# Optimization experiments

Hardware: AMD Instinct MI355X
Metric: run time of the kernel (lower is better)

Reference implementation:

```python
import jax, jax.numpy as jnp
import numpy as np


def setup_inputs() -> dict:
    key = jax.random.key(0)
    kK, kQ = jax.random.split(key)
    B, S, D = 8, 2048, 512
    K = jax.random.normal(kK, (B, S, D), dtype=jnp.float32)
    Q = jax.random.normal(kQ, (B, S, D), dtype=jnp.float32)
    return {"K": K, "Q": Q}


def reference(K, Q):
    # K: [B, S_k, D], Q: [B, S_q, D]
    S_q = Q.shape[1]
    S_k = K.shape[1]
    # Causal mask: -inf strictly above the diagonal (k=1), as in np.triu(..., k=1)
    mask = jnp.where(jnp.triu(jnp.ones((S_q, S_k), dtype=bool), k=1), -jnp.inf, 0.0).astype(jnp.float32)
    # NOTE: original scales by sqrt(window_size_keys) (seq len), and adds mask BEFORE scaling.
    logits = (jnp.einsum('bqd,bkd->bqk', Q, K) + mask) / jnp.sqrt(jnp.float32(S_k))
    return jax.nn.softmax(logits, axis=-1)
```

## Files before the change

### kernel.cpp

```cpp
#include <hip/hip_runtime.h>
#include <hip/hip_bf16.h>
#include <math.h>

#define B_SZ 8
#define SEQ 2048
#define DIM 512
#define NT (SEQ / 128)
#define NTRI (NT * (NT + 1) / 2)

typedef __attribute__((ext_vector_type(8))) short bf16x8;
typedef __attribute__((ext_vector_type(8))) unsigned short u16x8;
typedef __attribute__((ext_vector_type(4))) float f32x4;

#define GLOBAL_AS __attribute__((address_space(1)))
#define LDS_AS __attribute__((address_space(3)))

__device__ __forceinline__ unsigned short f2bf(float f) {
    unsigned int u = __builtin_bit_cast(unsigned int, f);
    u += 0x7fffu + ((u >> 16) & 1u);
    return (unsigned short)(u >> 16);
}

__device__ __forceinline__ void load_lds16(const void* g, void* l) {
    __builtin_amdgcn_global_load_lds((const GLOBAL_AS unsigned int*)g,
                                     (LDS_AS unsigned int*)l, 16, 0, 0);
}

__global__ __launch_bounds__(256)
void convert_kernel(const float* __restrict__ Qs, const float* __restrict__ Ks,
                    unsigned short* __restrict__ Qd, unsigned short* __restrict__ Kd) {
    const float* src = blockIdx.y ? Qs : Ks;
    unsigned short* dst = blockIdx.y ? Qd : Kd;
    const int base = blockIdx.x * (256 * 8) + threadIdx.x;
    const float4* s = (const float4*)src;
#pragma unroll
    for (int j = 0; j < 8; j++) {
        int i = base + j * 256;
        float4 a = s[2 * i];
        float4 b = s[2 * i + 1];
        u16x8 o;
        o[0] = f2bf(a.x); o[1] = f2bf(a.y); o[2] = f2bf(a.z); o[3] = f2bf(a.w);
        o[4] = f2bf(b.x); o[5] = f2bf(b.y); o[6] = f2bf(b.z); o[7] = f2bf(b.w);
        ((u16x8*)dst)[i] = o;
    }
}

#define BM 128
#define BK 32
__global__ __launch_bounds__(256)
void logits_exp(const unsigned short* __restrict__ Qb, const unsigned short* __restrict__ Kb,
                float* __restrict__ out, float* __restrict__ partials) {
    const int tid = blockIdx.x;
    const int b = blockIdx.y;
    int tq = (int)((sqrtf(8.f * (float)tid + 1.f) - 1.f) * 0.5f);
    while ((tq + 1) * (tq + 2) / 2 <= tid) tq++;
    while (tq * (tq + 1) / 2 > tid) tq--;
    const int tk = tid - tq * (tq + 1) / 2;

    __shared__ __align__(16) unsigned short a_lds[BM * BK];
    __shared__ __align__(16) unsigned short b_lds[BM * BK];

    const int t = threadIdx.x;
    const int wave = t >> 6;
    const int lane = t & 63;
    const int l16 = lane & 15;
    const int quad = lane >> 4;
    const int wm = wave >> 1;
    const int wn = wave & 1;

    const unsigned short* Qrow = Qb + ((size_t)b * SEQ + (size_t)tq * BM) * DIM;
    const unsigned short* Krow = Kb + ((size_t)b * SEQ + (size_t)tk * BM) * DIM;

    const int sr = lane >> 2;
    const int kg = lane & 3;

    f32x4 acc[4][4];
#pragma unroll
    for (int i = 0; i < 4; i++)
#pragma unroll
        for (int j = 0; j < 4; j++) acc[i][j] = (f32x4){0.f, 0.f, 0.f, 0.f};

    for (int k0 = 0; k0 < DIM; k0 += BK) {
#pragma unroll
        for (int j = wave; j < 8; j += 4) {
            int row = j * 16 + sr;
            load_lds16(Qrow + (size_t)row * DIM + k0 + kg * 8, &a_lds[(j * 16) * BK]);
            load_lds16(Krow + (size_t)row * DIM + k0 + kg * 8, &b_lds[(j * 16) * BK]);
        }
        __syncthreads();

        bf16x8 af[4], bf[4];
#pragma unroll
        for (int mi = 0; mi < 4; mi++)
            af[mi] = *(const bf16x8*)&a_lds[(wm * 64 + mi * 16 + l16) * BK + quad * 8];
#pragma unroll
        for (int ni = 0; ni < 4; ni++)
            bf[ni] = *(const bf16x8*)&b_lds[(wn * 64 + ni * 16 + l16) * BK + quad * 8];
#pragma unroll
        for (int mi = 0; mi < 4; mi++)
#pragma unroll
            for (int ni = 0; ni < 4; ni++)
                acc[mi][ni] = __builtin_amdgcn_mfma_f32_16x16x32_bf16(af[mi], bf[ni], acc[mi][ni], 0, 0, 0);
        __syncthreads();
    }

    const float scale = 0.02209708691207961f;
    const bool diag = (tk == tq);
    float* outb = out + (size_t)b * SEQ * SEQ;
#pragma unroll
    for (int mi = 0; mi < 4; mi++) {
        const int rowb = tq * BM + wm * 64 + mi * 16 + quad * 4;
#pragma unroll
        for (int r = 0; r < 4; r++) {
            const int row = rowb + r;
            float psum = 0.f;
#pragma unroll
            for (int ni = 0; ni < 4; ni++) {
                const int col = tk * BM + wn * 64 + ni * 16 + l16;
                float e = __expf(acc[mi][ni][r] * scale);
                e = (!diag || col <= row) ? e : 0.f;
                psum += e;
                outb[(size_t)row * SEQ + col] = e;
            }
            psum += __shfl_xor(psum, 1);
            psum += __shfl_xor(psum, 2);
            psum += __shfl_xor(psum, 4);
            psum += __shfl_xor(psum, 8);
            if (l16 == 0)
                partials[((size_t)b * SEQ + row) * 32 + tk * 2 + wn] = psum;
        }
    }
}

__global__ __launch_bounds__(256)
void rescale_kernel(float* __restrict__ out, const float* __restrict__ partials) {
    const int rowbase = blockIdx.x * 8;
    const int wave = threadIdx.x >> 6;
    const int lane = threadIdx.x & 63;
#pragma unroll
    for (int rr = 0; rr < 2; rr++) {
        const int grow = rowbase + wave * 2 + rr;
        const int q = grow & (SEQ - 1);
        const int tqt = q >> 7;
        const int nslots = (tqt + 1) * 2;
        float v = (lane < nslots) ? partials[(size_t)grow * 32 + lane] : 0.f;
        v += __shfl_xor(v, 1);
        v += __shfl_xor(v, 2);
        v += __shfl_xor(v, 4);
        v += __shfl_xor(v, 8);
        v += __shfl_xor(v, 16);
        v += __shfl_xor(v, 32);
        const float inv = 1.0f / v;
        const int n4 = (tqt + 1) * 32;
        float4* row = (float4*)(out + (size_t)grow * SEQ);
#pragma unroll
        for (int j = 0; j < 8; j++) {
            const int i = lane + j * 64;
            if (i < n4) {
                float4 e = row[i];
                e.x *= inv; e.y *= inv; e.z *= inv; e.w *= inv;
                row[i] = e;
            } else {
                row[i] = (float4){0.f, 0.f, 0.f, 0.f};
            }
        }
    }
}

extern "C" void kernel_launch(void* const* d_in, const int* in_sizes, int n_in,
                              void* d_out, int out_size, void* d_ws, size_t ws_size,
                              hipStream_t stream) {
    const float* Kp = (const float*)d_in[0];
    const float* Qp = (const float*)d_in[1];
    float* out = (float*)d_out;

    const size_t nElem = (size_t)B_SZ * SEQ * DIM;
    unsigned short* Qbf = (unsigned short*)d_ws;
    unsigned short* Kbf = Qbf + nElem;
    float* partials = (float*)(Kbf + nElem);

    convert_kernel<<<dim3(512, 2), dim3(256), 0, stream>>>(Qp, Kp, Qbf, Kbf);
    logits_exp<<<dim3(NTRI, B_SZ), dim3(256), 0, stream>>>(Qbf, Kbf, out, partials);
    rescale_kernel<<<dim3(B_SZ * SEQ / 8), dim3(256), 0, stream>>>(out, partials);
}
```

Before: 250.6 us.

## Double-buffer LDS in logits GEMM and batch loads in rescale kernel

The logits kernel now double-buffers its Q/K LDS tiles, issuing the next k-slice's global-to-LDS loads before computing on the current one. A partial vmcnt wait plus raw barriers replace the two full syncthreads per iteration, so memory latency can overlap with MFMA work. The rescale kernel issues all row loads for both rows before doing any multiplies and stores, which raises memory-level parallelism at the cost of more registers. The waitcnt encoding is hand-written and must match the number of outstanding loads; if it is wrong the kernel can read LDS before the data arrives.

Result: no change. 248.8 us (-0.7%).

```diff
diff --git a/kernel.cpp b/kernel.cpp
--- a/kernel.cpp
+++ b/kernel.cpp
@@ -57,8 +57,8 @@
     while (tq * (tq + 1) / 2 > tid) tq--;
     const int tk = tid - tq * (tq + 1) / 2;
 
-    __shared__ __align__(16) unsigned short a_lds[BM * BK];
-    __shared__ __align__(16) unsigned short b_lds[BM * BK];
+    __shared__ __align__(16) unsigned short a_lds[2][BM * BK];
+    __shared__ __align__(16) unsigned short b_lds[2][BM * BK];
 
     const int t = threadIdx.x;
     const int wave = t >> 6;
@@ -80,28 +80,43 @@
 #pragma unroll
         for (int j = 0; j < 4; j++) acc[i][j] = (f32x4){0.f, 0.f, 0.f, 0.f};
 
-    for (int k0 = 0; k0 < DIM; k0 += BK) {
-#pragma unroll
-        for (int j = wave; j < 8; j += 4) {
-            int row = j * 16 + sr;
-            load_lds16(Qrow + (size_t)row * DIM + k0 + kg * 8, &a_lds[(j * 16) * BK]);
-            load_lds16(Krow + (size_t)row * DIM + k0 + kg * 8, &b_lds[(j * 16) * BK]);
-        }
-        __syncthreads();
+    auto stage = [&](int k0, int buf) {
+#pragma unroll
+        for (int j = 0; j < 2; j++) {
+            int rg = (wave + 4 * j) * 16;
+            int row = rg + sr;
+            load_lds16(Qrow + (size_t)row * DIM + k0 + kg * 8, &a_lds[buf][rg * BK]);
+            load_lds16(Krow + (size_t)row * DIM + k0 + kg * 8, &b_lds[buf][rg * BK]);
+        }
+    };
+
+    stage(0, 0);
+    const int NITER = DIM / BK;
+    for (int k = 0; k < NITER; k++) {
+        const int buf = k & 1;
+        if (k + 1 < NITER) {
+            stage((k + 1) * BK, 1 - buf);
+            __builtin_amdgcn_s_waitcnt(0x0F74);
+            __builtin_amdgcn_s_barrier();
+        } else {
+            __syncthreads();
+        }
 
         bf16x8 af[4], bf[4];
 #pragma unroll
         for (int mi = 0; mi < 4; mi++)
-            af[mi] = *(const bf16x8*)&a_lds[(wm * 64 + mi * 16 + l16) * BK + quad * 8];
+            af[mi] = *(const bf16x8*)&a_lds[buf][(wm * 64 + mi * 16 + l16) * BK + quad * 8];
 #pragma unroll
         for (int ni = 0; ni < 4; ni++)
-            bf[ni] = *(const bf16x8*)&b_lds[(wn * 64 + ni * 16 + l16) * BK + quad * 8];
+            bf[ni] = *(const bf16x8*)&b_lds[buf][(wn * 64 + ni * 16 + l16) * BK + quad * 8];
 #pragma unroll
         for (int mi = 0; mi < 4; mi++)
 #pragma unroll
             for (int ni = 0; ni < 4; ni++)
                 acc[mi][ni] = __builtin_amdgcn_mfma_f32_16x16x32_bf16(af[mi], bf[ni], acc[mi][ni], 0, 0, 0);
-        __syncthreads();
+
+        if (k + 1 < NITER)
+            __builtin_amdgcn_s_barrier();
     }
 
     const float scale = 0.02209708691207961f;
@@ -137,32 +152,51 @@
     const int rowbase = blockIdx.x * 8;
     const int wave = threadIdx.x >> 6;
     const int lane = threadIdx.x & 63;
+    const int g0 = rowbase + wave * 2;
+
+    float inv[2];
+    int n4v[2];
 #pragma unroll
     for (int rr = 0; rr < 2; rr++) {
-        const int grow = rowbase + wave * 2 + rr;
+        const int grow = g0 + rr;
         const int q = grow & (SEQ - 1);
         const int tqt = q >> 7;
         const int nslots = (tqt + 1) * 2;
+        n4v[rr] = (tqt + 1) * 32;
         float v = (lane < nslots) ? partials[(size_t)grow * 32 + lane] : 0.f;
         v += __shfl_xor(v, 1);
         v += __shfl_xor(v, 2);
         v += __shfl_xor(v, 4);
         v += __shfl_xor(v, 8);
         v += __shfl_xor(v, 16);
-        v += __shfl_xor(v, 32);
-        const float inv = 1.0f / v;
-        const int n4 = (tqt + 1) * 32;
-        float4* row = (float4*)(out + (size_t)grow * SEQ);
+        inv[rr] = 1.0f / __shfl(v, 0);
+    }
+
+    float4 vals[2][8];
+#pragma unroll
+    for (int rr = 0; rr < 2; rr++) {
+        float4* row = (float4*)(out + (size_t)(g0 + rr) * SEQ);
 #pragma unroll
         for (int j = 0; j < 8; j++) {
             const int i = lane + j * 64;
-            if (i < n4) {
-                float4 e = row[i];
-                e.x *= inv; e.y *= inv; e.z *= inv; e.w *= inv;
-                row[i] = e;
+            if (i < n4v[rr]) vals[rr][j] = row[i];
+        }
+    }
+#pragma unroll
+    for (int rr = 0; rr < 2; rr++) {
+        float4* row = (float4*)(out + (size_t)(g0 + rr) * SEQ);
+        const float s = inv[rr];
+#pragma unroll
+        for (int j = 0; j < 8; j++) {
+            const int i = lane + j * 64;
+            float4 e;
+            if (i < n4v[rr]) {
+                e = vals[rr][j];
+                e.x *= s; e.y *= s; e.z *= s; e.w *= s;
             } else {
-                row[i] = (float4){0.f, 0.f, 0.f, 0.f};
+                e = (float4){0.f, 0.f, 0.f, 0.f};
             }
+            row[i] = e;
         }
     }
 }
```
